# Optimization experiments

Measured on AMD Instinct MI355X. Metric: run time of the kernel, lower is better.

Reference implementation:

```python
import jax, jax.numpy as jnp
import numpy as np

B, L, C, PS, K, NL, NH, DFF, MAXLEN = 64, 4096, 32, 16, 1024, 4, 8, 2048, 512
D = PS * C          # code_dim = 512
P = L // PS         # num_patches = 256
PA_H = 4            # heads in PatchCrossAttention (largest of {4,2,1} dividing C)
COMMIT = 0.25


def _ln(x, g, b, eps=1e-5):
    m = x.mean(-1, keepdims=True)
    v = x.var(-1, keepdims=True)
    return (x - m) / jnp.sqrt(v + eps) * g + b


def _mha(q, k, v, w_in, b_in, w_out, b_out, nh, mask=None):
    # torch nn.MultiheadAttention math: in_proj weight [3d, d], y = x @ W.T + b
    d = q.shape[-1]
    dh = d // nh
    wq, wk, wv = jnp.split(w_in, 3, axis=0)
    bq, bk, bv = jnp.split(b_in, 3, axis=0)
    qh = (q @ wq.T + bq).reshape(q.shape[0], q.shape[1], nh, dh)
    kh = (k @ wk.T + bk).reshape(k.shape[0], k.shape[1], nh, dh)
    vh = (v @ wv.T + bv).reshape(v.shape[0], v.shape[1], nh, dh)
    scores = jnp.einsum('bqhd,bkhd->bhqk', qh, kh) / jnp.sqrt(jnp.asarray(dh, q.dtype))
    if mask is not None:
        scores = jnp.where(mask, jnp.asarray(-jnp.inf, scores.dtype), scores)
    a = jax.nn.softmax(scores, axis=-1)
    o = jnp.einsum('bhqk,bkhd->bqhd', a, vh).reshape(q.shape[0], q.shape[1], d)
    return o @ w_out.T + b_out


def _forward(x, pa_lq, pa_pos, pa_win, pa_bin, pa_wout, pa_bout,
             pa_ln1g, pa_ln1b, pa_ln2g, pa_ln2b, pa_w1, pa_b1, pa_w2, pa_b2,
             cb, tf_pos, tf_win, tf_bin, tf_wout, tf_bout,
             tf_ln1g, tf_ln1b, tf_ln2g, tf_ln2b,
             tf_w1, tf_b1, tf_w2, tf_b2, fin_g, fin_b):
    Bx = x.shape[0]
    # --- patchify: [B, L, C] -> [B*P, PS, C] ---
    xp = x.reshape(Bx * P, PS, C)
    # --- PatchCrossAttention ---
    x_pos = xp + pa_pos                       # pos emb over patch steps
    lq = jnp.broadcast_to(pa_lq, xp.shape)    # learnable query tokens
    attn = _mha(lq, x_pos, x_pos, pa_win, pa_bin, pa_wout, pa_bout, PA_H)
    xn = _ln(lq + attn, pa_ln1g, pa_ln1b)
    f = jax.nn.gelu(xn @ pa_w1 + pa_b1, approximate=False) @ pa_w2 + pa_b2
    xo = _ln(xn + f, pa_ln2g, pa_ln2b)
    enc = xp + xo                             # residual to raw patch
    # --- flatten + VQ ---
    z = enc.reshape(Bx * P, D)
    d2 = (z * z).sum(1, keepdims=True) + (cb * cb).sum(1) - 2.0 * (z @ cb.T)
    idx = jnp.argmin(d2, axis=1)
    q = cb[idx]
    sg = jax.lax.stop_gradient
    e_loss = jnp.mean((sg(q) - z) ** 2)
    q_loss = jnp.mean((q - sg(z)) ** 2)
    vq_loss = q_loss + COMMIT * e_loss
    quant = z + sg(q - z)                     # straight-through
    # --- causal transformer over code sequence [B, P, D] ---
    t = quant.reshape(Bx, P, D) + tf_pos[:P]
    causal = jnp.triu(jnp.ones((P, P), dtype=bool), 1)
    for i in range(NL):  # post-LN TransformerEncoderLayer, gelu
        a = _mha(t, t, t, tf_win[i], tf_bin[i], tf_wout[i], tf_bout[i], NH, causal)
        t = _ln(t + a, tf_ln1g[i], tf_ln1b[i])
        f = jax.nn.gelu(t @ tf_w1[i] + tf_b1[i], approximate=False) @ tf_w2[i] + tf_b2[i]
        t = _ln(t + f, tf_ln2g[i], tf_ln2b[i])
    y = _ln(t, fin_g, fin_b)
    return y, vq_loss, idx


def setup_inputs() -> dict:
    key = jax.random.key(0)
    ks = iter(jax.random.split(key, 32))
    n = lambda shape, s=0.02: jax.random.normal(next(ks), shape, dtype=jnp.float32) * s
    inp = {
        'x': jax.random.normal(next(ks), (B, L, C), dtype=jnp.float32),
        'pa_lq': n((PS, C)), 'pa_pos': n((PS, C)),
        'pa_win': n((3 * C, C)), 'pa_bin': jnp.zeros((3 * C,), jnp.float32),
        'pa_wout': n((C, C)), 'pa_bout': jnp.zeros((C,), jnp.float32),
        'pa_ln1g': jnp.ones((C,), jnp.float32), 'pa_ln1b': jnp.zeros((C,), jnp.float32),
        'pa_ln2g': jnp.ones((C,), jnp.float32), 'pa_ln2b': jnp.zeros((C,), jnp.float32),
        'pa_w1': n((C, 2 * C)), 'pa_b1': jnp.zeros((2 * C,), jnp.float32),
        'pa_w2': n((2 * C, C)), 'pa_b2': jnp.zeros((C,), jnp.float32),
        'cb': jax.random.uniform(next(ks), (K, D), jnp.float32, -1.0 / K, 1.0 / K),
        'tf_pos': n((MAXLEN, D)),
        'tf_win': n((NL, 3 * D, D)), 'tf_bin': jnp.zeros((NL, 3 * D), jnp.float32),
        'tf_wout': n((NL, D, D)), 'tf_bout': jnp.zeros((NL, D), jnp.float32),
        'tf_ln1g': jnp.ones((NL, D), jnp.float32), 'tf_ln1b': jnp.zeros((NL, D), jnp.float32),
        'tf_ln2g': jnp.ones((NL, D), jnp.float32), 'tf_ln2b': jnp.zeros((NL, D), jnp.float32),
        'tf_w1': n((NL, D, DFF)), 'tf_b1': jnp.zeros((NL, DFF), jnp.float32),
        'tf_w2': n((NL, DFF, D)), 'tf_b2': jnp.zeros((NL, D), jnp.float32),
        'fin_g': jnp.ones((D,), jnp.float32), 'fin_b': jnp.zeros((D,), jnp.float32),
    }
    return inp


def reference(x, pa_lq, pa_pos, pa_win, pa_bin, pa_wout, pa_bout,
              pa_ln1g, pa_ln1b, pa_ln2g, pa_ln2b, pa_w1, pa_b1, pa_w2, pa_b2,
              cb, tf_pos, tf_win, tf_bin, tf_wout, tf_bout,
              tf_ln1g, tf_ln1b, tf_ln2g, tf_ln2b,
              tf_w1, tf_b1, tf_w2, tf_b2, fin_g, fin_b):
    return _forward(x, pa_lq, pa_pos, pa_win, pa_bin, pa_wout, pa_bout,
                    pa_ln1g, pa_ln1b, pa_ln2g, pa_ln2b, pa_w1, pa_b1, pa_w2, pa_b2,
                    cb, tf_pos, tf_win, tf_bin, tf_wout, tf_bout,
                    tf_ln1g, tf_ln1b, tf_ln2g, tf_ln2b,
                    tf_w1, tf_b1, tf_w2, tf_b2, fin_g, fin_b)
```

## Files before the change

### kernel.cpp

```cpp
#include <hip/hip_runtime.h>


#define SQRT1_2F 0.70710678118654752440f

typedef __attribute__((ext_vector_type(8))) short short8;
typedef __attribute__((ext_vector_type(4))) float f32x4;
typedef __attribute__((ext_vector_type(8))) unsigned short ushort8;
typedef unsigned short ushort;
typedef unsigned long long u64;

__device__ __forceinline__ float gelu_exact(float v) {
  return 0.5f * v * (1.0f + erff(v * SQRT1_2F));
}

__device__ __forceinline__ ushort f2b_rne(float f) {
  unsigned u = __float_as_uint(f);
  unsigned r = (u + 0x7fffu + ((u >> 16) & 1u)) >> 16;
  return (ushort)r;
}

__device__ __forceinline__ float b2f(ushort u) {
  return __uint_as_float(((unsigned)u) << 16);
}

__device__ __forceinline__ void gload16(const void* g, void* l) {
  __builtin_amdgcn_global_load_lds(
      (const __attribute__((address_space(1))) void*)g,
      (__attribute__((address_space(3))) void*)l, 16, 0, 0);
}

__device__ __forceinline__ unsigned fkey(float d) {
  unsigned u = __float_as_uint(d);
  return (u & 0x80000000u) ? ~u : (u | 0x80000000u);
}

__global__ __launch_bounds__(64) void patch_setup_kernel(
    const float* __restrict__ lq, const float* __restrict__ win,
    const float* __restrict__ bin, const float* __restrict__ w1,
    const float* __restrict__ w2, float* __restrict__ q16,
    float* __restrict__ w1T, float* __restrict__ w2T) {
  const int tid = threadIdx.x;
#pragma unroll
  for (int q = 0; q < 8; q++) {
    int e = tid + (q << 6);
    int i = e >> 5, c = e & 31;
    const float* wr = win + (size_t)c * 32;
    float acc = bin[c];
#pragma unroll
    for (int d = 0; d < 32; d++) acc += lq[(i << 5) + d] * wr[d];
    q16[e] = acc;
  }
#pragma unroll
  for (int q = 0; q < 32; q++) {
    int e = tid + (q << 6);
    int u = e >> 5, d = e & 31;
    w1T[e] = w1[(size_t)d * 64 + u];
  }
#pragma unroll
  for (int q = 0; q < 32; q++) {
    int e = tid + (q << 6);
    int c = e >> 6, u = e & 63;
    w2T[e] = w2[(size_t)u * 32 + c];
  }
}

__device__ __forceinline__ void ln_16xS(float* buf, const float* g,
                                        const float* bb, int tid) {
  int row = tid >> 2, sub = tid & 3;
  int c0 = sub << 3;
  float* r = buf + row * 34 + c0;
  float v[8];
  float s = 0.f, s2 = 0.f;
#pragma unroll
  for (int n = 0; n < 8; n++) {
    float t = r[n];
    v[n] = t; s += t; s2 += t * t;
  }
  s += __shfl_xor(s, 1);  s += __shfl_xor(s, 2);
  s2 += __shfl_xor(s2, 1); s2 += __shfl_xor(s2, 2);
  float m = s * (1.0f / 32.0f);
  float var = s2 * (1.0f / 32.0f) - m * m;
  float inv = 1.0f / sqrtf(var + 1e-5f);
#pragma unroll
  for (int n = 0; n < 8; n++)
    r[n] = (v[n] - m) * inv * g[c0 + n] + bb[c0 + n];
}

__global__ __launch_bounds__(256) void pkA_kernel(
    const float* __restrict__ x, const float* __restrict__ pos,
    const float* __restrict__ win, const float* __restrict__ bin,
    const float* __restrict__ q16, float* __restrict__ so) {
  __shared__ float sxp[2048];
  __shared__ float skv[4096];
  __shared__ float sq16[16 * 33];
  const int blk = blockIdx.x, t = threadIdx.x;
  const int p0 = blk << 2;
  const int cfix = t & 31;

#pragma unroll
  for (int q = 0; q < 8; q++) {
    int e = t + (q << 8);
    int pl = e >> 9, r = e & 511;
    sxp[e] = x[(size_t)(p0 + pl) * 512 + r] + pos[r];
  }
  if (t < 128) {
#pragma unroll
    for (int q = 0; q < 4; q++) {
      int e = t + (q << 7);
      sq16[(e >> 5) * 33 + (e & 31)] = q16[e];
    }
  }

  float wr0[32], wr1[32];
#pragma unroll
  for (int d4 = 0; d4 < 8; d4++) {
    *(float4*)(wr0 + 4 * d4) =
        *(const float4*)(win + (size_t)(32 + cfix) * 32 + 4 * d4);
    *(float4*)(wr1 + 4 * d4) =
        *(const float4*)(win + (size_t)(64 + cfix) * 32 + 4 * d4);
  }
  const float bk = bin[32 + cfix];
  const float bv = bin[64 + cfix];
  __syncthreads();

#pragma unroll
  for (int q = 0; q < 16; q++) {
    int e = t + (q << 8);
    int pl = e >> 10, rr = e & 1023;
    int w = rr >> 9, rj = rr & 511, j = rj >> 5;
    const float* sx = sxp + (pl << 9) + (j << 5);
    const float* wreg = w ? wr1 : wr0;
    float acc = w ? bv : bk;
#pragma unroll
    for (int d = 0; d < 32; d++) acc += sx[d] * wreg[d];
    skv[e] = acc;
  }
  __syncthreads();

  const int pl = t >> 6, hh = (t >> 4) & 3, i = t & 15;
  const int p = p0 + pl;
  const float* kp = skv + (pl << 10);
  const int hd = hh << 3;

  float sc[16];
#pragma unroll
  for (int j = 0; j < 16; j++) {
    float acc = 0.f;
#pragma unroll
    for (int d = 0; d < 8; d++)
      acc += sq16[i * 33 + hd + d] * kp[(j << 5) + hd + d];
    sc[j] = acc * 0.35355339059327373f;
  }
  {
    float mx = sc[0];
#pragma unroll
    for (int j = 1; j < 16; j++) mx = fmaxf(mx, sc[j]);
    float sm = 0.f;
    float ev[16];
#pragma unroll
    for (int j = 0; j < 16; j++) { ev[j] = expf(sc[j] - mx); sm += ev[j]; }
    float inv = 1.0f / sm;
#pragma unroll
    for (int j = 0; j < 16; j++) sc[j] = ev[j] * inv;
  }
  float* orow = so + (size_t)p * 512 + (i << 5) + hd;
#pragma unroll
  for (int c8 = 0; c8 < 8; c8++) {
    const int c = hd + c8;
    float acc = 0.f;
#pragma unroll
    for (int j = 0; j < 16; j++) acc += sc[j] * kp[512 + (j << 5) + c];
    orow[c8] = acc;
  }
}

__global__ __launch_bounds__(64) void pkB_kernel(
    const float* __restrict__ so_g, const float* __restrict__ x,
    const float* __restrict__ wout, const float* __restrict__ bout,
    const float* __restrict__ lq,
    const float* __restrict__ ln1g, const float* __restrict__ ln1b,
    const float* __restrict__ w1T, const float* __restrict__ b1,
    const float* __restrict__ w2T, const float* __restrict__ b2,
    const float* __restrict__ ln2g, const float* __restrict__ ln2b,
    float* __restrict__ z, ushort* __restrict__ zh,
    ushort* __restrict__ zl, float* __restrict__ znorm) {
  __shared__ float sso[544], sst[544], ssh[1056];
  const int p = blockIdx.x, t = threadIdx.x;
  const int cfix = t & 31;

#pragma unroll
  for (int q = 0; q < 8; q++) {
    int e = t + (q << 6);
    sso[(e >> 5) * 34 + (e & 31)] = so_g[(size_t)p * 512 + e];
  }

  float wo[32];
#pragma unroll
  for (int d4 = 0; d4 < 8; d4++)
    *(float4*)(wo + 4 * d4) = *(const float4*)(wout + (size_t)cfix * 32 + 4 * d4);
  __syncthreads();

#pragma unroll
  for (int q = 0; q < 8; q++) {
    int e = t + (q << 6);
    int i = e >> 5;
    float acc = bout[cfix];
#pragma unroll
    for (int d = 0; d < 32; d++) acc += sso[i * 34 + d] * wo[d];
    sst[i * 34 + cfix] = acc + lq[(i << 5) + cfix];
  }
  __syncthreads();
  ln_16xS(sst, ln1g, ln1b, t);

  float w1r[32];
#pragma unroll
  for (int d4 = 0; d4 < 8; d4++)
    *(float4*)(w1r + 4 * d4) = *(const float4*)(w1T + (size_t)t * 32 + 4 * d4);
  __syncthreads();

#pragma unroll
  for (int q = 0; q < 16; q++) {
    int i = q;
    float acc = b1[t];
#pragma unroll
    for (int d = 0; d < 32; d++) acc += sst[i * 34 + d] * w1r[d];
    ssh[i * 66 + t] = gelu_exact(acc);
  }

  float w2r[64];
#pragma unroll
  for (int u4 = 0; u4 < 16; u4++)
    *(float4*)(w2r + 4 * u4) = *(const float4*)(w2T + (size_t)cfix * 64 + 4 * u4);
  __syncthreads();

#pragma unroll
  for (int q = 0; q < 8; q++) {
    int e = t + (q << 6);
    int i = e >> 5;
    float acc = b2[cfix];
#pragma unroll
    for (int u = 0; u < 64; u++) acc += ssh[i * 66 + u] * w2r[u];
    sso[i * 34 + cfix] = acc + sst[i * 34 + cfix];
  }
  __syncthreads();
  ln_16xS(sso, ln2g, ln2b, t);
  __syncthreads();

  const float* xp = x + (size_t)p * 512;
  const int row = t >> 2, c0v = (t & 3) << 3;
  float zv[8];
#pragma unroll
  for (int n = 0; n < 8; n++)
    zv[n] = xp[(t << 3) + n] + sso[row * 34 + c0v + n];
  float* zo = z + (size_t)p * 512 + (t << 3);
  *(float4*)(zo)     = *(float4*)(zv);
  *(float4*)(zo + 4) = *(float4*)(zv + 4);
  ushort8 hv, lv;
  float s2 = 0.f;
#pragma unroll
  for (int n = 0; n < 8; n++) {
    s2 += zv[n] * zv[n];
    ushort h = f2b_rne(zv[n]);
    hv[n] = h;
    lv[n] = f2b_rne(zv[n] - b2f(h));
  }
  *(ushort8*)(zh + (size_t)p * 512 + (t << 3)) = hv;
  *(ushort8*)(zl + (size_t)p * 512 + (t << 3)) = lv;
#pragma unroll
  for (int off = 1; off < 64; off <<= 1) s2 += __shfl_xor(s2, off);
  if (t == 0) znorm[p] = s2;
}

__global__ __launch_bounds__(64) void cbnorm_kernel(
    const float* __restrict__ cb, float* __restrict__ cbn,
    ushort* __restrict__ ch, ushort* __restrict__ cl) {
  int c = blockIdx.x, lane = threadIdx.x;
  const float* r = cb + (size_t)c * 512 + lane * 8;
  float v[8];
  *(float4*)(v)     = *(const float4*)(r);
  *(float4*)(v + 4) = *(const float4*)(r + 4);
  float s = 0.f;
  ushort8 hv, lv;
#pragma unroll
  for (int n = 0; n < 8; n++) {
    s += v[n] * v[n];
    ushort h = f2b_rne(v[n]);
    hv[n] = h;
    lv[n] = f2b_rne(v[n] - b2f(h));
  }
  *(ushort8*)(ch + (size_t)c * 512 + lane * 8) = hv;
  *(ushort8*)(cl + (size_t)c * 512 + lane * 8) = lv;
#pragma unroll
  for (int off = 1; off < 64; off <<= 1) s += __shfl_xor(s, off);
  if (lane == 0) cbn[c] = s;
}

__global__ __launch_bounds__(256) void gemm_vq_b3(
    const ushort* __restrict__ Ah, const ushort* __restrict__ Al,
    const ushort* __restrict__ Bh, const ushort* __restrict__ Bl,
    const float* __restrict__ znorm, const float* __restrict__ cbn,
    u64* __restrict__ packed) {
  __shared__ ushort sAh[4096], sAl[4096], sBh[4096], sBl[4096];
  const int cpx = gridDim.x >> 3;
  const int bid = (blockIdx.x & 7) * cpx + (blockIdx.x >> 3);
  const int bx = bid & 7, by = bid >> 3;
  const int m0 = by << 7, n0 = bx << 7;
  const int tid = threadIdx.x;
  const int wid = tid >> 6, lane = tid & 63;
  const int wr = wid >> 1, wc = wid & 1;
  const int l15 = lane & 15, lk = lane >> 4;

  const f32x4 fzero = {0.f, 0.f, 0.f, 0.f};
  f32x4 acc[4][4];
#pragma unroll
  for (int i = 0; i < 4; i++)
#pragma unroll
    for (int j = 0; j < 4; j++) acc[i][j] = fzero;

  for (int k0 = 0; k0 < 512; k0 += 32) {
#pragma unroll
    for (int c = 0; c < 2; c++) {
      const int I = tid + (c << 8);
      const int r = I >> 2, kk = (I & 3) << 3;
      const size_t ga = (size_t)(m0 + r) * 512 + k0 + kk;
      const size_t gb = (size_t)(n0 + r) * 512 + k0 + kk;
      const size_t lo = (size_t)((wid << 6) + (c << 8)) * 8;
      gload16(Ah + ga, sAh + lo);
      gload16(Al + ga, sAl + lo);
      gload16(Bh + gb, sBh + lo);
      gload16(Bl + gb, sBl + lo);
    }
    __syncthreads();

    short8 ah[4], al[4], bh[4], bl[4];
#pragma unroll
    for (int m = 0; m < 4; m++) {
      const int ar = ((wr << 6) + (m << 4) + l15) * 32 + lk * 8;
      ah[m] = *(const short8*)(sAh + ar);
      al[m] = *(const short8*)(sAl + ar);
      const int br = ((wc << 6) + (m << 4) + l15) * 32 + lk * 8;
      bh[m] = *(const short8*)(sBh + br);
      bl[m] = *(const short8*)(sBl + br);
    }
#pragma unroll
    for (int m = 0; m < 4; m++)
#pragma unroll
      for (int n = 0; n < 4; n++) {
        acc[m][n] = __builtin_amdgcn_mfma_f32_16x16x32_bf16(ah[m], bh[n],
                                                            acc[m][n], 0, 0, 0);
        acc[m][n] = __builtin_amdgcn_mfma_f32_16x16x32_bf16(ah[m], bl[n],
                                                            acc[m][n], 0, 0, 0);
        acc[m][n] = __builtin_amdgcn_mfma_f32_16x16x32_bf16(al[m], bh[n],
                                                            acc[m][n], 0, 0, 0);
      }
    __syncthreads();
  }

  float zn[4][4];
#pragma unroll
  for (int m = 0; m < 4; m++)
#pragma unroll
    for (int r = 0; r < 4; r++)
      zn[m][r] = znorm[m0 + (wr << 6) + (m << 4) + (lk << 2) + r];
  float cbnv[4];
#pragma unroll
  for (int n = 0; n < 4; n++)
    cbnv[n] = cbn[n0 + (wc << 6) + (n << 4) + l15];

#pragma unroll
  for (int m = 0; m < 4; m++) {
#pragma unroll
    for (int r = 0; r < 4; r++) {
      u64 best = ~0ull;
#pragma unroll
      for (int n = 0; n < 4; n++) {
        const int gcol = n0 + (wc << 6) + (n << 4) + l15;
        float d = (zn[m][r] + cbnv[n]) - 2.0f * acc[m][n][r];
        u64 key = ((u64)fkey(d) << 32) | (unsigned)gcol;
        best = best < key ? best : key;
      }
#pragma unroll
      for (int off = 1; off < 16; off <<= 1) {
        u64 o = __shfl_xor(best, off);
        best = best < o ? best : o;
      }
      if (l15 == 0) {
        const int grow = m0 + (wr << 6) + (m << 4) + (lk << 2) + r;
        atomicMin(&packed[grow], best);
      }
    }
  }
}

__global__ __launch_bounds__(256) void vq_slim_kernel(
    const u64* __restrict__ packed, const float* __restrict__ cb,
    const float* __restrict__ z, const float* __restrict__ tf_pos,
    float* __restrict__ t, ushort* __restrict__ th,
    float* __restrict__ idx_out, float* __restrict__ loss_part) {
  __shared__ float spart[4];
  const int wv = threadIdx.x >> 6;
  const int r = (blockIdx.x << 2) + wv;
  const int lane = threadIdx.x & 63;
  const int bi = (int)(unsigned)(packed[r] & 0xFFFFFFFFull);
  const float* zr = z + (size_t)r * 512 + (lane << 3);
  const float* q = cb + (size_t)bi * 512 + (lane << 3);
  const float* pr = tf_pos + (size_t)(r & 255) * 512 + (lane << 3);
  float zv[8], qv[8], pv[8];
  *(float4*)(zv)     = *(const float4*)(zr);
  *(float4*)(zv + 4) = *(const float4*)(zr + 4);
  *(float4*)(qv)     = *(const float4*)(q);
  *(float4*)(qv + 4) = *(const float4*)(q + 4);
  *(float4*)(pv)     = *(const float4*)(pr);
  *(float4*)(pv + 4) = *(const float4*)(pr + 4);
  float lsum = 0.f;
  float tv[8];
  ushort8 w;
#pragma unroll
  for (int n = 0; n < 8; n++) {
    float diff = qv[n] - zv[n];
    lsum += diff * diff;
    tv[n] = qv[n] + pv[n];
    w[n] = f2b_rne(tv[n]);
  }
  float* to = t + (size_t)r * 512 + (lane << 3);
  *(float4*)(to)     = *(float4*)(tv);
  *(float4*)(to + 4) = *(float4*)(tv + 4);
  *(ushort8*)(th + (size_t)r * 512 + (lane << 3)) = w;
#pragma unroll
  for (int off = 1; off < 64; off <<= 1) lsum += __shfl_xor(lsum, off);
  if (lane == 0) {
    idx_out[r] = (float)bi;
    spart[wv] = lsum;
  }
  __syncthreads();
  if (threadIdx.x == 0)
    loss_part[blockIdx.x] = (spart[0] + spart[1]) + (spart[2] + spart[3]);
}

__global__ __launch_bounds__(256) void loss_reduce_kernel(
    const float* __restrict__ loss_part, float* __restrict__ loss_out) {
  __shared__ float sw[4];
  float s = 0.f;
  for (int i = threadIdx.x; i < 4096; i += 256) s += loss_part[i];
#pragma unroll
  for (int off = 1; off < 64; off <<= 1) s += __shfl_xor(s, off);
  const int wv = threadIdx.x >> 6;
  if ((threadIdx.x & 63) == 0) sw[wv] = s;
  __syncthreads();
  if (threadIdx.x == 0)
    loss_out[0] = ((sw[0] + sw[1]) + (sw[2] + sw[3])) * (1.25f / 8388608.0f);
}

template <int OUTMODE>
__global__ __launch_bounds__(256) void gemm_bf16_kernel(
    const ushort* __restrict__ A, const ushort* __restrict__ B,
    const float* __restrict__ bias, void* __restrict__ Cout,
    int M, int N, int K) {
  __shared__ ushort As[8192];
  __shared__ ushort Bs[8192];
  const int nbx = N >> 7;
  const int cpx = gridDim.x >> 3;
  const int bid = (blockIdx.x & 7) * cpx + (blockIdx.x >> 3);
  const int bx = bid % nbx, by = bid / nbx;
  const int m0 = by << 7, n0 = bx << 7;
  const int tid = threadIdx.x;
  const int wid = tid >> 6, lane = tid & 63;
  const int wr = wid >> 1, wc = wid & 1;
  const int l15 = lane & 15, lk = lane >> 4;

  const f32x4 fzero = {0.f, 0.f, 0.f, 0.f};
  f32x4 acc[4][4];
#pragma unroll
  for (int i = 0; i < 4; i++)
#pragma unroll
    for (int j = 0; j < 4; j++) acc[i][j] = fzero;

  for (int k0 = 0; k0 < K; k0 += 64) {
#pragma unroll
    for (int c = 0; c < 4; c++) {
      const int base = (c << 8) + (wid << 6);
      const int half = base >> 9;
      const int Jb = base & 511;
      const int J = Jb + lane;
      const int r = J >> 2, kk = (J & 3) << 3;
      gload16(A + (size_t)(m0 + r) * K + k0 + (half << 5) + kk,
              As + (size_t)((half << 12) + Jb * 8));
      gload16(B + (size_t)(n0 + r) * K + k0 + (half << 5) + kk,
              Bs + (size_t)((half << 12) + Jb * 8));
    }
    __syncthreads();

#pragma unroll
    for (int kc = 0; kc < 2; kc++) {
      short8 a[4], b[4];
#pragma unroll
      for (int m = 0; m < 4; m++) {
        const int ar = (kc << 12) + ((wr << 6) + (m << 4) + l15) * 32 + lk * 8;
        a[m] = *(const short8*)(As + ar);
        const int br = (kc << 12) + ((wc << 6) + (m << 4) + l15) * 32 + lk * 8;
        b[m] = *(const short8*)(Bs + br);
      }
#pragma unroll
      for (int m = 0; m < 4; m++)
#pragma unroll
        for (int n = 0; n < 4; n++)
          acc[m][n] = __builtin_amdgcn_mfma_f32_16x16x32_bf16(a[m], b[n],
                                                              acc[m][n], 0, 0, 0);
    }
    __syncthreads();
  }

  float bv[4];
#pragma unroll
  for (int n = 0; n < 4; n++)
    bv[n] = bias[n0 + (wc << 6) + (n << 4) + l15];

#pragma unroll
  for (int m = 0; m < 4; m++) {
#pragma unroll
    for (int n = 0; n < 4; n++) {
      const int gcol = n0 + (wc << 6) + (n << 4) + l15;
#pragma unroll
      for (int r = 0; r < 4; r++) {
        const int grow = m0 + (wr << 6) + (m << 4) + (lk << 2) + r;
        float v = acc[m][n][r] + bv[n];
        if (OUTMODE == 0) {
          ((float*)Cout)[(size_t)grow * N + gcol] = v;
        } else if (OUTMODE == 1) {
          ((ushort*)Cout)[(size_t)grow * N + gcol] = f2b_rne(gelu_exact(v));
        } else {
          ((ushort*)Cout)[(size_t)grow * N + gcol] = f2b_rne(v);
        }
      }
    }
  }
}

__global__ void cvt_flat(const float* __restrict__ in, ushort* __restrict__ out,
                         int n) {
  int i = blockIdx.x * blockDim.x + threadIdx.x;
  const int stride = gridDim.x * blockDim.x;
  for (; i < n; i += stride) out[i] = f2b_rne(in[i]);
}

__global__ __launch_bounds__(256) void cvt_tr(const float* __restrict__ in,
                                              ushort* __restrict__ out,
                                              int R, int C) {
  __shared__ float tile[32][33];
  const int bc = blockIdx.x, br = blockIdx.y, lay = blockIdx.z;
  const float* src = in + (size_t)lay * R * C;
  ushort* dst = out + (size_t)lay * R * C;
  const int tid = threadIdx.x;
#pragma unroll
  for (int q = 0; q < 4; q++) {
    int idx = tid + (q << 8);
    int rr = idx >> 5, cc = idx & 31;
    tile[rr][cc] = src[(size_t)(br * 32 + rr) * C + bc * 32 + cc];
  }
  __syncthreads();
#pragma unroll
  for (int q = 0; q < 4; q++) {
    int idx = tid + (q << 8);
    int co = idx >> 5, ro = idx & 31;
    dst[(size_t)(bc * 32 + co) * R + br * 32 + ro] = f2b_rne(tile[ro][co]);
  }
}

__global__ __launch_bounds__(64) void attn_mfma_kernel(
    const ushort* __restrict__ qkv, ushort* __restrict__ o) {
  __shared__ ushort lds[8192];
  char* KsB = (char*)lds;
  char* VtB = (char*)(lds + 4096);
  const int bid = blockIdx.x;
  const int xcd = bid & 7, slot = bid >> 3;
  const int b = (xcd << 3) | (slot >> 5);
  const int h = (slot >> 2) & 7;
  const int qb = slot & 3;
  const int lane = threadIdx.x;
  const int l15 = lane & 15, lk4 = lane >> 4;

  short8 qf[4][2];
#pragma unroll
  for (int m = 0; m < 4; m++)
#pragma unroll
    for (int kc = 0; kc < 2; kc++)
      qf[m][kc] = *(const short8*)(qkv +
          (size_t)(b * 256 + qb * 64 + m * 16 + l15) * 1536 +
          h * 64 + kc * 32 + lk4 * 8);

  const f32x4 fz = {0.f, 0.f, 0.f, 0.f};
  f32x4 O[4][4];
#pragma unroll
  for (int m = 0; m < 4; m++)
#pragma unroll
    for (int n = 0; n < 4; n++) O[m][n] = fz;
  float lsum[4][4];
#pragma unroll
  for (int m = 0; m < 4; m++)
#pragma unroll
    for (int r = 0; r < 4; r++) lsum[m][r] = 0.f;

  ushort8 kv[8], vv[8];
  {
    const ushort* krow = qkv + (size_t)(b * 256 + lane) * 1536 + 512 + h * 64;
#pragma unroll
    for (int u = 0; u < 8; u++) kv[u] = ((const ushort8*)krow)[u];
#pragma unroll
    for (int u = 0; u < 8; u++) vv[u] = ((const ushort8*)(krow + 512))[u];
  }

  for (int jt = 0; jt <= qb; jt++) {
    __syncthreads();
    {
      const int rx = (lane & 7) << 4;
#pragma unroll
      for (int u = 0; u < 8; u++)
        *(ushort8*)(KsB + lane * 128 + ((u << 4) ^ rx)) = kv[u];
#pragma unroll
      for (int u = 0; u < 8; u++)
#pragma unroll
        for (int i = 0; i < 8; i++) {
          const int d = u * 8 + i;
          *(ushort*)(VtB + ((d * 128 + lane * 2) ^ ((d & 7) << 4))) =
              (ushort)vv[u][i];
        }
    }
    __syncthreads();

    if (jt < qb) {
      const ushort* krow = qkv +
          (size_t)(b * 256 + (jt + 1) * 64 + lane) * 1536 + 512 + h * 64;
#pragma unroll
      for (int u = 0; u < 8; u++) kv[u] = ((const ushort8*)krow)[u];
#pragma unroll
      for (int u = 0; u < 8; u++) vv[u] = ((const ushort8*)(krow + 512))[u];
    }

    f32x4 sacc[4][4];
#pragma unroll
    for (int m = 0; m < 4; m++)
#pragma unroll
      for (int n = 0; n < 4; n++) sacc[m][n] = fz;
    __builtin_amdgcn_s_setprio(1);
#pragma unroll
    for (int kc = 0; kc < 2; kc++) {
      short8 bf[4];
#pragma unroll
      for (int n = 0; n < 4; n++) {
        const int row = n * 16 + l15;
        bf[n] = *(const short8*)(KsB + row * 128 +
                                 ((kc * 64 + lk4 * 16) ^ ((row & 7) << 4)));
      }
#pragma unroll
      for (int m = 0; m < 4; m++)
#pragma unroll
        for (int n = 0; n < 4; n++)
          sacc[m][n] = __builtin_amdgcn_mfma_f32_16x16x32_bf16(
              qf[m][kc], bf[n], sacc[m][n], 0, 0, 0);
    }
    __builtin_amdgcn_s_setprio(0);
    __syncthreads();

    const bool diag = (jt == qb);
#pragma unroll
    for (int m = 0; m < 4; m++)
#pragma unroll
      for (int n = 0; n < 4; n++)
#pragma unroll
        for (int r = 0; r < 4; r++) {
          const int ql = m * 16 + lk4 * 4 + r;
          const int jl = n * 16 + l15;
          float e = __expf(sacc[m][n][r] * 0.125f);
          if (diag && jl > ql) e = 0.f;
          const ushort pu = f2b_rne(e);
          lsum[m][r] += b2f(pu);
          *(ushort*)(KsB + ql * 128 + ((jl * 2) ^ ((ql & 7) << 4))) = pu;
        }
    __syncthreads();

    __builtin_amdgcn_s_setprio(1);
#pragma unroll
    for (int kc = 0; kc < 2; kc++) {
      short8 pf[4], vf[4];
#pragma unroll
      for (int m = 0; m < 4; m++) {
        const int row = m * 16 + l15;
        pf[m] = *(const short8*)(KsB + row * 128 +
                                 ((kc * 64 + lk4 * 16) ^ ((row & 7) << 4)));
      }
#pragma unroll
      for (int n = 0; n < 4; n++) {
        const int row = n * 16 + l15;
        vf[n] = *(const short8*)(VtB + row * 128 +
                                 ((kc * 64 + lk4 * 16) ^ ((row & 7) << 4)));
      }
#pragma unroll
      for (int m = 0; m < 4; m++)
#pragma unroll
        for (int n = 0; n < 4; n++)
          O[m][n] = __builtin_amdgcn_mfma_f32_16x16x32_bf16(
              pf[m], vf[n], O[m][n], 0, 0, 0);
    }
    __builtin_amdgcn_s_setprio(0);
  }

  float inv[4][4];
#pragma unroll
  for (int m = 0; m < 4; m++)
#pragma unroll
    for (int r = 0; r < 4; r++) {
      float v = lsum[m][r];
      v += __shfl_xor(v, 1); v += __shfl_xor(v, 2);
      v += __shfl_xor(v, 4); v += __shfl_xor(v, 8);
      inv[m][r] = 1.0f / v;
    }
#pragma unroll
  for (int m = 0; m < 4; m++)
#pragma unroll
    for (int n = 0; n < 4; n++)
#pragma unroll
      for (int r = 0; r < 4; r++) {
        const int row = b * 256 + qb * 64 + m * 16 + lk4 * 4 + r;
        const int col = h * 64 + n * 16 + l15;
        o[(size_t)row * 512 + col] = f2b_rne(O[m][n][r] * inv[m][r]);
      }
}

__global__ __launch_bounds__(256) void ln_kernel(
    const float* __restrict__ xin, const ushort* __restrict__ addin_b,
    const float* __restrict__ g, const float* __restrict__ bb,
    float* __restrict__ outp, ushort* __restrict__ outb) {
  const int r = blockIdx.x * 4 + (threadIdx.x >> 6);
  const int lane = threadIdx.x & 63;
  const float* xr = xin + (size_t)r * 512 + lane * 8;
  float v[8];
  *(float4*)(v)     = *(const float4*)(xr);
  *(float4*)(v + 4) = *(const float4*)(xr + 4);
  if (addin_b) {
    ushort8 a = *(const ushort8*)(addin_b + (size_t)r * 512 + lane * 8);
#pragma unroll
    for (int n = 0; n < 8; n++) v[n] += b2f(a[n]);
  }
  float s = 0.f, s2 = 0.f;
#pragma unroll
  for (int n = 0; n < 8; n++) { s += v[n]; s2 += v[n] * v[n]; }
#pragma unroll
  for (int off = 1; off < 64; off <<= 1) {
    s += __shfl_xor(s, off);
    s2 += __shfl_xor(s2, off);
  }
  float m = s * (1.0f / 512.0f);
  float var = s2 * (1.0f / 512.0f) - m * m;
  float inv = 1.0f / sqrtf(var + 1e-5f);
  const int c0 = lane * 8;
  float outv[8];
#pragma unroll
  for (int n = 0; n < 8; n++) outv[n] = (v[n] - m) * inv * g[c0 + n] + bb[c0 + n];
  float* orow = outp + (size_t)r * 512 + c0;
  *(float4*)(orow)     = *(float4*)(outv);
  *(float4*)(orow + 4) = *(float4*)(outv + 4);
  if (outb) {
    ushort8 w;
#pragma unroll
    for (int n = 0; n < 8; n++) w[n] = f2b_rne(outv[n]);
    *(ushort8*)(outb + (size_t)r * 512 + c0) = w;
  }
}

extern "C" void kernel_launch(void* const* d_in, const int* in_sizes, int n_in,
                              void* d_out, int out_size, void* d_ws, size_t ws_size,
                              hipStream_t stream) {
  const float* x       = (const float*)d_in[0];
  const float* pa_lq   = (const float*)d_in[1];
  const float* pa_pos  = (const float*)d_in[2];
  const float* pa_win  = (const float*)d_in[3];
  const float* pa_bin  = (const float*)d_in[4];
  const float* pa_wout = (const float*)d_in[5];
  const float* pa_bout = (const float*)d_in[6];
  const float* pa_ln1g = (const float*)d_in[7];
  const float* pa_ln1b = (const float*)d_in[8];
  const float* pa_ln2g = (const float*)d_in[9];
  const float* pa_ln2b = (const float*)d_in[10];
  const float* pa_w1   = (const float*)d_in[11];
  const float* pa_b1   = (const float*)d_in[12];
  const float* pa_w2   = (const float*)d_in[13];
  const float* pa_b2   = (const float*)d_in[14];
  const float* cb      = (const float*)d_in[15];
  const float* tf_pos  = (const float*)d_in[16];
  const float* tf_win  = (const float*)d_in[17];
  const float* tf_bin  = (const float*)d_in[18];
  const float* tf_wout = (const float*)d_in[19];
  const float* tf_bout = (const float*)d_in[20];
  const float* tf_ln1g = (const float*)d_in[21];
  const float* tf_ln1b = (const float*)d_in[22];
  const float* tf_ln2g = (const float*)d_in[23];
  const float* tf_ln2b = (const float*)d_in[24];
  const float* tf_w1   = (const float*)d_in[25];
  const float* tf_b1   = (const float*)d_in[26];
  const float* tf_w2   = (const float*)d_in[27];
  const float* tf_b2   = (const float*)d_in[28];
  const float* fin_g   = (const float*)d_in[29];
  const float* fin_b   = (const float*)d_in[30];

  float* yout = (float*)d_out;
  float* loss_out = yout + 8388608;
  float* idx_out = loss_out + 1;

  float* ws   = (float*)d_ws;
  float* z    = ws;
  float* tb   = z + 8388608;
  float* bufA = tb + 8388608;
  float* bufC = bufA + 16777216;
  float* wreg = bufC + 8388608;
  float* treg = wreg + 6291456;
  float* cbn  = treg + 4194304;
  float* q16  = cbn + 1024;
  float* w1T  = q16 + 512;
  float* w2T  = w1T + 2048;
  float* znorm = w2T + 2048;
  u64*   packed = (u64*)(znorm + 16384);
  float* loss_part = (float*)(packed + 16384);

  ushort* win_b  = (ushort*)wreg;
  ushort* wout_b = win_b + 3145728;
  ushort* w1t_b  = wout_b + 1048576;
  ushort* w2t_b  = w1t_b + 4194304;
  ushort* tbh    = (ushort*)treg;
  ushort* qkvh   = (ushort*)bufA;
  ushort* abh    = (ushort*)z;
  ushort* zh_b   = (ushort*)bufC;
  ushort* zl_b   = zh_b + 8388608;
  ushort* projh  = (ushort*)bufC;
  ushort* ch_b   = (ushort*)treg;
  ushort* cl_b   = ch_b + 524288;

  hipMemsetAsync(packed, 0xFF, 16384 * sizeof(u64), stream);
  cbnorm_kernel<<<1024, 64, 0, stream>>>(cb, cbn, ch_b, cl_b);
  patch_setup_kernel<<<1, 64, 0, stream>>>(pa_lq, pa_win, pa_bin, pa_w1,
                                           pa_w2, q16, w1T, w2T);

  pkA_kernel<<<4096, 256, 0, stream>>>(x, pa_pos, pa_win, pa_bin, q16, bufA);
  pkB_kernel<<<16384, 64, 0, stream>>>(bufA, x, pa_wout, pa_bout, pa_lq,
                                       pa_ln1g, pa_ln1b, w1T, pa_b1,
                                       w2T, pa_b2, pa_ln2g, pa_ln2b, z,
                                       zh_b, zl_b, znorm);

  cvt_flat<<<2048, 256, 0, stream>>>(tf_win, win_b, 3145728);
  cvt_flat<<<1024, 256, 0, stream>>>(tf_wout, wout_b, 1048576);
  cvt_tr<<<dim3(64, 16, 4), 256, 0, stream>>>(tf_w1, w1t_b, 512, 2048);
  cvt_tr<<<dim3(16, 64, 4), 256, 0, stream>>>(tf_w2, w2t_b, 2048, 512);

  gemm_vq_b3<<<dim3(1024), 256, 0, stream>>>(zh_b, zl_b, ch_b, cl_b,
                                             znorm, cbn, packed);
  vq_slim_kernel<<<4096, 256, 0, stream>>>(packed, cb, z, tf_pos, tb, tbh,
                                           idx_out, loss_part);
  loss_reduce_kernel<<<1, 256, 0, stream>>>(loss_part, loss_out);

  for (int l = 0; l < 4; l++) {
    gemm_bf16_kernel<2><<<dim3(128 * 12), 256, 0, stream>>>(
        tbh, win_b + (size_t)l * 1536 * 512, tf_bin + l * 1536, qkvh,
        16384, 1536, 512);
    attn_mfma_kernel<<<dim3(2048), 64, 0, stream>>>(qkvh, abh);
    gemm_bf16_kernel<2><<<dim3(128 * 4), 256, 0, stream>>>(
        abh, wout_b + (size_t)l * 512 * 512, tf_bout + l * 512, projh,
        16384, 512, 512);
    ln_kernel<<<dim3(4096), 256, 0, stream>>>(tb, projh, tf_ln1g + l * 512,
                                              tf_ln1b + l * 512, tb, tbh);
    gemm_bf16_kernel<1><<<dim3(128 * 16), 256, 0, stream>>>(
        tbh, w1t_b + (size_t)l * 1048576, tf_b1 + l * 2048, qkvh,
        16384, 2048, 512);
    gemm_bf16_kernel<2><<<dim3(128 * 4), 256, 0, stream>>>(
        qkvh, w2t_b + (size_t)l * 1048576, tf_b2 + l * 512, projh,
        16384, 512, 2048);
    ln_kernel<<<dim3(4096), 256, 0, stream>>>(tb, projh, tf_ln2g + l * 512,
                                              tf_ln2b + l * 512, tb, tbh);
  }
  ln_kernel<<<dim3(4096), 256, 0, stream>>>(tb, nullptr, fin_g, fin_b, yout,
                                            nullptr);

  (void)in_sizes; (void)n_in; (void)out_size; (void)ws_size;
}
```

Before: 1.303 ms.

## Fuse patch cross-attention and MLP kernels into one kernel

Merges pkA (K/V projection and attention) and pkB (out-projection, LN, MLP, LN, residual, VQ prep) into a single kernel with 4 patches per block. Each wave then handles one patch for the second stage, and shared memory is reused across the two phases. This removes the global round trip of the attention output (a 32MB write and read) and one launch. The cost is more shared memory per block, which may lower occupancy, plus extra block-wide barriers.

```diff
diff --git a/kernel.cpp b/kernel.cpp
--- a/kernel.cpp
+++ b/kernel.cpp
@@ -86,96 +86,10 @@
     r[n] = (v[n] - m) * inv * g[c0 + n] + bb[c0 + n];
 }
 
-__global__ __launch_bounds__(256) void pkA_kernel(
+__global__ __launch_bounds__(256) void pkF_kernel(
     const float* __restrict__ x, const float* __restrict__ pos,
     const float* __restrict__ win, const float* __restrict__ bin,
-    const float* __restrict__ q16, float* __restrict__ so) {
-  __shared__ float sxp[2048];
-  __shared__ float skv[4096];
-  __shared__ float sq16[16 * 33];
-  const int blk = blockIdx.x, t = threadIdx.x;
-  const int p0 = blk << 2;
-  const int cfix = t & 31;
-
-#pragma unroll
-  for (int q = 0; q < 8; q++) {
-    int e = t + (q << 8);
-    int pl = e >> 9, r = e & 511;
-    sxp[e] = x[(size_t)(p0 + pl) * 512 + r] + pos[r];
-  }
-  if (t < 128) {
-#pragma unroll
-    for (int q = 0; q < 4; q++) {
-      int e = t + (q << 7);
-      sq16[(e >> 5) * 33 + (e & 31)] = q16[e];
-    }
-  }
-
-  float wr0[32], wr1[32];
-#pragma unroll
-  for (int d4 = 0; d4 < 8; d4++) {
-    *(float4*)(wr0 + 4 * d4) =
-        *(const float4*)(win + (size_t)(32 + cfix) * 32 + 4 * d4);
-    *(float4*)(wr1 + 4 * d4) =
-        *(const float4*)(win + (size_t)(64 + cfix) * 32 + 4 * d4);
-  }
-  const float bk = bin[32 + cfix];
-  const float bv = bin[64 + cfix];
-  __syncthreads();
-
-#pragma unroll
-  for (int q = 0; q < 16; q++) {
-    int e = t + (q << 8);
-    int pl = e >> 10, rr = e & 1023;
-    int w = rr >> 9, rj = rr & 511, j = rj >> 5;
-    const float* sx = sxp + (pl << 9) + (j << 5);
-    const float* wreg = w ? wr1 : wr0;
-    float acc = w ? bv : bk;
-#pragma unroll
-    for (int d = 0; d < 32; d++) acc += sx[d] * wreg[d];
-    skv[e] = acc;
-  }
-  __syncthreads();
-
-  const int pl = t >> 6, hh = (t >> 4) & 3, i = t & 15;
-  const int p = p0 + pl;
-  const float* kp = skv + (pl << 10);
-  const int hd = hh << 3;
-
-  float sc[16];
-#pragma unroll
-  for (int j = 0; j < 16; j++) {
-    float acc = 0.f;
-#pragma unroll
-    for (int d = 0; d < 8; d++)
-      acc += sq16[i * 33 + hd + d] * kp[(j << 5) + hd + d];
-    sc[j] = acc * 0.35355339059327373f;
-  }
-  {
-    float mx = sc[0];
-#pragma unroll
-    for (int j = 1; j < 16; j++) mx = fmaxf(mx, sc[j]);
-    float sm = 0.f;
-    float ev[16];
-#pragma unroll
-    for (int j = 0; j < 16; j++) { ev[j] = expf(sc[j] - mx); sm += ev[j]; }
-    float inv = 1.0f / sm;
-#pragma unroll
-    for (int j = 0; j < 16; j++) sc[j] = ev[j] * inv;
-  }
-  float* orow = so + (size_t)p * 512 + (i << 5) + hd;
-#pragma unroll
-  for (int c8 = 0; c8 < 8; c8++) {
-    const int c = hd + c8;
-    float acc = 0.f;
-#pragma unroll
-    for (int j = 0; j < 16; j++) acc += sc[j] * kp[512 + (j << 5) + c];
-    orow[c8] = acc;
-  }
-}
-
-__global__ __launch_bounds__(64) void pkB_kernel(
-    const float* __restrict__ so_g, const float* __restrict__ x,
+    const float* __restrict__ q16,
     const float* __restrict__ wout, const float* __restrict__ bout,
     const float* __restrict__ lq,
     const float* __restrict__ ln1g, const float* __restrict__ ln1b,
@@ -184,47 +98,132 @@
     const float* __restrict__ ln2g, const float* __restrict__ ln2b,
     float* __restrict__ z, ushort* __restrict__ zh,
     ushort* __restrict__ zl, float* __restrict__ znorm) {
-  __shared__ float sso[544], sst[544], ssh[1056];
-  const int p = blockIdx.x, t = threadIdx.x;
+  __shared__ float sso[2176];
+  __shared__ float ubuf[6672];
+  float* sxp  = ubuf;
+  float* skv  = ubuf + 2048;
+  float* sq16 = ubuf + 6144;
+  float* sstA = ubuf;
+  float* sshA = ubuf + 2176;
+
+  const int blk = blockIdx.x, t = threadIdx.x;
+  const int p0 = blk << 2;
   const int cfix = t & 31;
+  const int wv = t >> 6, lane = t & 63;
 
 #pragma unroll
   for (int q = 0; q < 8; q++) {
-    int e = t + (q << 6);
-    sso[(e >> 5) * 34 + (e & 31)] = so_g[(size_t)p * 512 + e];
-  }
+    int e = t + (q << 8);
+    int pl = e >> 9, r = e & 511;
+    sxp[e] = x[(size_t)(p0 + pl) * 512 + r] + pos[r];
+  }
+  if (t < 128) {
+#pragma unroll
+    for (int q = 0; q < 4; q++) {
+      int e = t + (q << 7);
+      sq16[(e >> 5) * 33 + (e & 31)] = q16[e];
+    }
+  }
+
+  float wr0[32], wr1[32];
+#pragma unroll
+  for (int d4 = 0; d4 < 8; d4++) {
+    *(float4*)(wr0 + 4 * d4) =
+        *(const float4*)(win + (size_t)(32 + cfix) * 32 + 4 * d4);
+    *(float4*)(wr1 + 4 * d4) =
+        *(const float4*)(win + (size_t)(64 + cfix) * 32 + 4 * d4);
+  }
+  const float bk = bin[32 + cfix];
+  const float bvv = bin[64 + cfix];
+  __syncthreads();
+
+#pragma unroll
+  for (int q = 0; q < 16; q++) {
+    int e = t + (q << 8);
+    int pl = e >> 10, rr = e & 1023;
+    int w = rr >> 9, rj = rr & 511, j = rj >> 5;
+    const float* sx = sxp + (pl << 9) + (j << 5);
+    const float* wreg = w ? wr1 : wr0;
+    float acc = w ? bvv : bk;
+#pragma unroll
+    for (int d = 0; d < 32; d++) acc += sx[d] * wreg[d];
+    skv[e] = acc;
+  }
+  __syncthreads();
+
+  {
+    const int pl = t >> 6, hh = (t >> 4) & 3, i = t & 15;
+    const float* kp = skv + (pl << 10);
+    const int hd = hh << 3;
+
+    float sc[16];
+#pragma unroll
+    for (int j = 0; j < 16; j++) {
+      float acc = 0.f;
+#pragma unroll
+      for (int d = 0; d < 8; d++)
+        acc += sq16[i * 33 + hd + d] * kp[(j << 5) + hd + d];
+      sc[j] = acc * 0.35355339059327373f;
+    }
+    {
+      float mx = sc[0];
+#pragma unroll
+      for (int j = 1; j < 16; j++) mx = fmaxf(mx, sc[j]);
+      float sm = 0.f;
+      float ev[16];
+#pragma unroll
+      for (int j = 0; j < 16; j++) { ev[j] = expf(sc[j] - mx); sm += ev[j]; }
+      float inv = 1.0f / sm;
+#pragma unroll
+      for (int j = 0; j < 16; j++) sc[j] = ev[j] * inv;
+    }
+    float* orow = sso + pl * 544 + i * 34 + hd;
+#pragma unroll
+    for (int c8 = 0; c8 < 8; c8++) {
+      const int c = hd + c8;
+      float acc = 0.f;
+#pragma unroll
+      for (int j = 0; j < 16; j++) acc += sc[j] * kp[512 + (j << 5) + c];
+      orow[c8] = acc;
+    }
+  }
+  __syncthreads();
+
+  const int p = p0 + wv;
+  float* psso = sso + wv * 544;
+  float* psst = sstA + wv * 544;
+  float* pssh = sshA + wv * 1056;
 
   float wo[32];
 #pragma unroll
   for (int d4 = 0; d4 < 8; d4++)
     *(float4*)(wo + 4 * d4) = *(const float4*)(wout + (size_t)cfix * 32 + 4 * d4);
-  __syncthreads();
 
 #pragma unroll
   for (int q = 0; q < 8; q++) {
-    int e = t + (q << 6);
+    int e = lane + (q << 6);
     int i = e >> 5;
     float acc = bout[cfix];
 #pragma unroll
-    for (int d = 0; d < 32; d++) acc += sso[i * 34 + d] * wo[d];
-    sst[i * 34 + cfix] = acc + lq[(i << 5) + cfix];
-  }
-  __syncthreads();
-  ln_16xS(sst, ln1g, ln1b, t);
+    for (int d = 0; d < 32; d++) acc += psso[i * 34 + d] * wo[d];
+    psst[i * 34 + cfix] = acc + lq[(i << 5) + cfix];
+  }
+  __syncthreads();
+  ln_16xS(psst, ln1g, ln1b, lane);
 
   float w1r[32];
 #pragma unroll
   for (int d4 = 0; d4 < 8; d4++)
-    *(float4*)(w1r + 4 * d4) = *(const float4*)(w1T + (size_t)t * 32 + 4 * d4);
+    *(float4*)(w1r + 4 * d4) = *(const float4*)(w1T + (size_t)lane * 32 + 4 * d4);
   __syncthreads();
 
 #pragma unroll
   for (int q = 0; q < 16; q++) {
     int i = q;
-    float acc = b1[t];
-#pragma unroll
-    for (int d = 0; d < 32; d++) acc += sst[i * 34 + d] * w1r[d];
-    ssh[i * 66 + t] = gelu_exact(acc);
+    float acc = b1[lane];
+#pragma unroll
+    for (int d = 0; d < 32; d++) acc += psst[i * 34 + d] * w1r[d];
+    pssh[i * 66 + lane] = gelu_exact(acc);
   }
 
   float w2r[64];
@@ -235,24 +234,24 @@
 
 #pragma unroll
   for (int q = 0; q < 8; q++) {
-    int e = t + (q << 6);
+    int e = lane + (q << 6);
     int i = e >> 5;
     float acc = b2[cfix];
 #pragma unroll
-    for (int u = 0; u < 64; u++) acc += ssh[i * 66 + u] * w2r[u];
-    sso[i * 34 + cfix] = acc + sst[i * 34 + cfix];
-  }
-  __syncthreads();
-  ln_16xS(sso, ln2g, ln2b, t);
+    for (int u = 0; u < 64; u++) acc += pssh[i * 66 + u] * w2r[u];
+    psso[i * 34 + cfix] = acc + psst[i * 34 + cfix];
+  }
+  __syncthreads();
+  ln_16xS(psso, ln2g, ln2b, lane);
   __syncthreads();
 
   const float* xp = x + (size_t)p * 512;
-  const int row = t >> 2, c0v = (t & 3) << 3;
+  const int row = lane >> 2, c0v = (lane & 3) << 3;
   float zv[8];
 #pragma unroll
   for (int n = 0; n < 8; n++)
-    zv[n] = xp[(t << 3) + n] + sso[row * 34 + c0v + n];
-  float* zo = z + (size_t)p * 512 + (t << 3);
+    zv[n] = xp[(lane << 3) + n] + psso[row * 34 + c0v + n];
+  float* zo = z + (size_t)p * 512 + (lane << 3);
   *(float4*)(zo)     = *(float4*)(zv);
   *(float4*)(zo + 4) = *(float4*)(zv + 4);
   ushort8 hv, lv;
@@ -264,11 +263,11 @@
     hv[n] = h;
     lv[n] = f2b_rne(zv[n] - b2f(h));
   }
-  *(ushort8*)(zh + (size_t)p * 512 + (t << 3)) = hv;
-  *(ushort8*)(zl + (size_t)p * 512 + (t << 3)) = lv;
+  *(ushort8*)(zh + (size_t)p * 512 + (lane << 3)) = hv;
+  *(ushort8*)(zl + (size_t)p * 512 + (lane << 3)) = lv;
 #pragma unroll
   for (int off = 1; off < 64; off <<= 1) s2 += __shfl_xor(s2, off);
-  if (t == 0) znorm[p] = s2;
+  if (lane == 0) znorm[p] = s2;
 }
 
 __global__ __launch_bounds__(64) void cbnorm_kernel(
@@ -839,11 +838,11 @@
   patch_setup_kernel<<<1, 64, 0, stream>>>(pa_lq, pa_win, pa_bin, pa_w1,
                                            pa_w2, q16, w1T, w2T);
 
-  pkA_kernel<<<4096, 256, 0, stream>>>(x, pa_pos, pa_win, pa_bin, q16, bufA);
-  pkB_kernel<<<16384, 64, 0, stream>>>(bufA, x, pa_wout, pa_bout, pa_lq,
+  pkF_kernel<<<4096, 256, 0, stream>>>(x, pa_pos, pa_win, pa_bin, q16,
+                                       pa_wout, pa_bout, pa_lq,
                                        pa_ln1g, pa_ln1b, w1T, pa_b1,
-                                       w2T, pa_b2, pa_ln2g, pa_ln2b, z,
-                                       zh_b, zl_b, znorm);
+                                       w2T, pa_b2, pa_ln2g, pa_ln2b,
+                                       z, zh_b, zl_b, znorm);
 
   cvt_flat<<<2048, 256, 0, stream>>>(tf_win, win_b, 3145728);
   cvt_flat<<<1024, 256, 0, stream>>>(tf_wout, wout_b, 1048576);
```

Measured after the change: 1.302 ms. About the same (-0.1%).
